# Performance work log

Measured on AMD Instinct MI355X. Metric: run time of the kernel, lower is better.

Reference implementation:

```python
import jax, jax.numpy as jnp
import numpy as np

N_FREQ = 12
NUM_LODS = 8
NUM_SAMPLED_LODS = 1
N_NEURONS = 64
OUT_CH = 11  # NUM_CANONICAL_CHANNELS = sum([3,3,1,1,1,1,1])
LRELU_SLOPE = 0.01
B = 1 << 20
# base_res = max_resolution >> (n_levels - 1); fpl = save_bits // quantize_bits = 4
GRIDS = [dict(base_res=16, n_levels=8, fpl=4),   # max_res 2048
         dict(base_res=16, n_levels=7, fpl=4)]   # max_res 1024


def _level_geom(base_res, level):
    # tcnn dense grid: scale = base_res * 2^level - 1, res = ceil(scale) + 1
    scale = base_res * (2.0 ** level) - 1.0
    res = int(np.ceil(scale)) + 1
    return res, scale


def _grid_n_params(g):
    return sum(_level_geom(g['base_res'], l)[0] ** 2 for l in range(g['n_levels'])) * g['fpl']


def triangle_wave(uv, n_freq):
    # tcnn TriangleWave: per dim, per frequency f: tri(x * 2^f), dim-major layout
    freqs = (2.0 ** jnp.arange(n_freq, dtype=jnp.float32))
    xf = uv[:, :, None] * freqs                      # [B, 2, F]
    t = jnp.abs(xf - jnp.floor(xf + 0.5)) * 4.0 - 1.0
    return t.reshape(uv.shape[0], -1)                # [B, 2*F]


def dense_grid_encode(uv, params_flat, base_res, n_levels, fpl):
    # Multi-level dense grid with bilinear interpolation (tcnn Grid/Dense/Linear).
    feats = []
    offset = 0
    for level in range(n_levels):
        res, scale = _level_geom(base_res, level)
        n = res * res * fpl
        table = params_flat[offset:offset + n].reshape(res * res, fpl)
        offset += n
        pos = uv * scale + 0.5                       # [B, 2]
        p0f = jnp.floor(pos)
        w = pos - p0f                                # bilinear weights
        p0 = jnp.clip(p0f.astype(jnp.int32), 0, res - 1)
        p1 = jnp.minimum(p0 + 1, res - 1)
        ix0, iy0 = p0[:, 0], p0[:, 1]
        ix1, iy1 = p1[:, 0], p1[:, 1]
        # tcnn index stride: dim0 fastest -> idx = ix + iy*res
        f00 = table[iy0 * res + ix0]
        f10 = table[iy0 * res + ix1]
        f01 = table[iy1 * res + ix0]
        f11 = table[iy1 * res + ix1]
        wx = w[:, 0:1]
        wy = w[:, 1:2]
        f = (f00 * (1 - wx) + f10 * wx) * (1 - wy) + (f01 * (1 - wx) + f11 * wx) * wy
        feats.append(f)                              # [B, fpl]
    return jnp.concatenate(feats, axis=1)            # [B, n_levels*fpl], level-major


def _forward(x, grid0_params, grid1_params, W_in, W_h, W_out):
    uvs = jnp.remainder(x[:, 0:2], 1.0)
    lod = x[:, 2:3]
    mips = lod * (NUM_LODS - NUM_SAMPLED_LODS)       # [B, 1]
    pe = triangle_wave(uvs, N_FREQ)                  # [B, 24]
    feats = []
    for g, params in zip(GRIDS, [grid0_params, grid1_params]):
        L, F = g['n_levels'], g['fpl']
        allf = dense_grid_encode(uvs, params, g['base_res'], L, F)  # [B, L*F]
        clipped = jnp.minimum(mips, float(L - NUM_SAMPLED_LODS))
        cols = ((L - NUM_SAMPLED_LODS - clipped) * F
                + jnp.arange(F * NUM_SAMPLED_LODS, dtype=jnp.float32)).astype(jnp.int32)
        feats.append(jnp.take_along_axis(allf, cols, axis=1))       # [B, F]
    inp = jnp.concatenate([pe] + feats + [lod], axis=1)             # [B, 33]
    lrelu = lambda h: jnp.where(h > 0, h, LRELU_SLOPE * h)
    h = lrelu(inp @ W_in)
    h = lrelu(h @ W_h)
    return lrelu(h @ W_out)                          # [B, 11]


def setup_inputs() -> dict:
    key = jax.random.key(0)
    ks = jax.random.split(key, 6)
    x = jax.random.uniform(ks[0], (B, 3), dtype=jnp.float32)
    grid0 = jax.random.uniform(ks[1], (_grid_n_params(GRIDS[0]),), jnp.float32, -0.1, 0.1)
    grid1 = jax.random.uniform(ks[2], (_grid_n_params(GRIDS[1]),), jnp.float32, -0.1, 0.1)
    n_in = N_FREQ * 2 + sum(g['fpl'] for g in GRIDS) * NUM_SAMPLED_LODS + 1
    W_in = jax.random.normal(ks[3], (n_in, N_NEURONS), jnp.float32) / np.float32(np.sqrt(n_in))
    W_h = jax.random.normal(ks[4], (N_NEURONS, N_NEURONS), jnp.float32) / np.float32(np.sqrt(N_NEURONS))
    W_out = jax.random.normal(ks[5], (N_NEURONS, OUT_CH), jnp.float32) / np.float32(np.sqrt(N_NEURONS))
    return dict(x=x, grid0_params=grid0, grid1_params=grid1, W_in=W_in, W_h=W_h, W_out=W_out)


def reference(x, grid0_params, grid1_params, W_in, W_h, W_out):
    return _forward(x, grid0_params, grid1_params, W_in, W_h, W_out)
```

## Files before the change

kernel.cpp:

```cpp
#include <hip/hip_runtime.h>

typedef float f32x4 __attribute__((ext_vector_type(4)));
typedef __bf16 bf16x8 __attribute__((ext_vector_type(8)));

#define PERM __builtin_amdgcn_perm

static __device__ __forceinline__ bf16x8 as_bf(uint4 v) {
    union { uint4 u; bf16x8 b; } c; c.u = v; return c.b;
}

static __device__ __forceinline__ float lrelu(float x) { return x > 0.0f ? x : 0.01f * x; }

static __device__ __forceinline__ unsigned pack_hilo(float v) {
    unsigned b = __float_as_uint(v);
    unsigned hi = (b + 0x7FFFu + ((b >> 16) & 1u)) >> 16;
    float hif = __uint_as_float(hi << 16);
    float lof = v - hif;
    unsigned lb = __float_as_uint(lof);
    unsigned lo = (lb + 0x7FFFu + ((lb >> 16) & 1u)) >> 16;
    return (hi << 16) | lo;
}

static __device__ __forceinline__ void unpack_frag(uint4 p0, uint4 p1, uint4& hi, uint4& lo) {
    hi.x = PERM(p0.y, p0.x, 0x07060302u);
    hi.y = PERM(p0.w, p0.z, 0x07060302u);
    hi.z = PERM(p1.y, p1.x, 0x07060302u);
    hi.w = PERM(p1.w, p1.z, 0x07060302u);
    lo.x = PERM(p0.y, p0.x, 0x05040100u);
    lo.y = PERM(p0.w, p0.z, 0x05040100u);
    lo.z = PERM(p1.y, p1.x, 0x05040100u);
    lo.w = PERM(p1.w, p1.z, 0x05040100u);
}

static __device__ __forceinline__ void read_frag_w(const unsigned* q, uint4& hi, uint4& lo) {
    uint4 p0 = *(const uint4*)(q);
    uint4 p1 = *(const uint4*)(q + 4);
    unpack_frag(p0, p1, hi, lo);
}

static __device__ __forceinline__ void read_frag_a(const unsigned* actb, int r, int kbase, int g,
                                                   uint4& hi, uint4& lo) {
    const unsigned* row = actb + r * 64;
    int cb = (kbase >> 2) + 2 * g;
    int rx = r & 15;
    uint4 p0 = *(const uint4*)(row + ((cb ^ rx) << 2));
    uint4 p1 = *(const uint4*)(row + (((cb + 1) ^ rx) << 2));
    unpack_frag(p0, p1, hi, lo);
}

static __device__ __forceinline__ void act_store(unsigned* actb, int row, int col, unsigned val) {
    int pos = row * 64 + ((((col >> 2) ^ (row & 15)) << 2) | (col & 3));
    actb[pos] = val;
}

static __device__ __forceinline__ f32x4 mfma3(const uint4& ah, const uint4& al,
                                              const uint4& bh, const uint4& bl, f32x4 c) {
    c = __builtin_amdgcn_mfma_f32_16x16x32_bf16(as_bf(ah), as_bf(bh), c, 0, 0, 0);
    c = __builtin_amdgcn_mfma_f32_16x16x32_bf16(as_bf(al), as_bf(bh), c, 0, 0, 0);
    c = __builtin_amdgcn_mfma_f32_16x16x32_bf16(as_bf(ah), as_bf(bl), c, 0, 0, 0);
    return c;
}

static __device__ __forceinline__ void issue_level(const float4* __restrict__ tbl, float u, float v,
                                                   int l, float4 r[4], float& wx, float& wy) {
    const int res = 16 << l;
    const float scale = (float)(res - 1);
    float px = u * scale + 0.5f;
    float py = v * scale + 0.5f;
    float fx = floorf(px), fy = floorf(py);
    wx = px - fx; wy = py - fy;
    int ix0 = min(max((int)fx, 0), res - 1);
    int iy0 = min(max((int)fy, 0), res - 1);
    int ix1 = min(ix0 + 1, res - 1);
    int iy1 = min(iy0 + 1, res - 1);
    unsigned base = (0x55555555u & ((1u << (2 * l)) - 1u)) * 256u;
    r[0] = tbl[base + iy0 * res + ix0];
    r[1] = tbl[base + iy0 * res + ix1];
    r[2] = tbl[base + iy1 * res + ix0];
    r[3] = tbl[base + iy1 * res + ix1];
}

static __device__ __forceinline__ void gather_issue(const float4* __restrict__ tbl, float u, float v,
                                                    float mips, float Lm1,
                                                    float4 r[8], float w[4], int cols[4]) {
    float clipped = fminf(mips, Lm1);
    float c0 = (Lm1 - clipped) * 4.0f;
    asm volatile("" : "+v"(c0));
    cols[0] = (int)c0;
    cols[1] = (int)(c0 + 1.0f);
    cols[2] = (int)(c0 + 2.0f);
    cols[3] = (int)(c0 + 3.0f);
    int lA = cols[0] >> 2;
    int lB = cols[3] >> 2;
    issue_level(tbl, u, v, lA, &r[0], w[0], w[1]);
    issue_level(tbl, u, v, lB, &r[4], w[2], w[3]);
}

static __device__ __forceinline__ void gather_finish(const float4 r[8], const float w[4],
                                                     const int cols[4], float out[4]) {
    float A[4], Bv[4];
    {
        float owx = 1.0f - w[0], owy = 1.0f - w[1];
        A[0] = (r[0].x * owx + r[1].x * w[0]) * owy + (r[2].x * owx + r[3].x * w[0]) * w[1];
        A[1] = (r[0].y * owx + r[1].y * w[0]) * owy + (r[2].y * owx + r[3].y * w[0]) * w[1];
        A[2] = (r[0].z * owx + r[1].z * w[0]) * owy + (r[2].z * owx + r[3].z * w[0]) * w[1];
        A[3] = (r[0].w * owx + r[1].w * w[0]) * owy + (r[2].w * owx + r[3].w * w[0]) * w[1];
    }
    {
        float owx = 1.0f - w[2], owy = 1.0f - w[3];
        Bv[0] = (r[4].x * owx + r[5].x * w[2]) * owy + (r[6].x * owx + r[7].x * w[2]) * w[3];
        Bv[1] = (r[4].y * owx + r[5].y * w[2]) * owy + (r[6].y * owx + r[7].y * w[2]) * w[3];
        Bv[2] = (r[4].z * owx + r[5].z * w[2]) * owy + (r[6].z * owx + r[7].z * w[2]) * w[3];
        Bv[3] = (r[4].w * owx + r[5].w * w[2]) * owy + (r[6].w * owx + r[7].w * w[2]) * w[3];
    }
    int lA = cols[0] >> 2;
    #pragma unroll
    for (int j = 0; j < 4; ++j) {
        int lj = cols[j] >> 2;
        int fj = cols[j] & 3;
        float va = A[0];
        va = (fj == 1) ? A[1] : va;
        va = (fj == 2) ? A[2] : va;
        va = (fj == 3) ? A[3] : va;
        float vb = Bv[0];
        vb = (fj == 1) ? Bv[1] : vb;
        vb = (fj == 2) ? Bv[2] : vb;
        vb = (fj == 3) ? Bv[3] : vb;
        out[j] = (lj == lA) ? va : vb;
    }
}

static __device__ __forceinline__ void pe_compute(float coord, unsigned pep[12]) {
    #pragma unroll
    for (int f = 0; f < 12; ++f) {
        float fr = (float)(1 << f);
        float xf = coord * fr;
        float t = fabsf(xf - floorf(xf + 0.5f)) * 4.0f - 1.0f;
        pep[f] = pack_hilo(t);
    }
}

#define LDS_U32 (2048 + 4096 + 1024 + 64 + 128 + 8192)

__global__ __launch_bounds__(256, 2) void tcnn_fwd(
    const float* __restrict__ x,
    const float4* __restrict__ g0,
    const float4* __restrict__ g1,
    const float* __restrict__ Win,
    const float* __restrict__ Wh,
    const float* __restrict__ Wout,
    float* __restrict__ out,
    int npts)
{
    extern __shared__ unsigned smem[];
    unsigned* s_winT  = smem;
    unsigned* s_whT   = s_winT + 2048;
    unsigned* s_woutT = s_whT + 4096;
    float*    s_lodw  = (float*)(s_woutT + 1024);
    float*    s_lodv  = s_lodw + 64;
    unsigned* s_act   = (unsigned*)(s_lodv + 128);

    const int tid = threadIdx.x;

    for (int e = tid; e < 2048; e += 256) {
        int n = e >> 5, k = e & 31;
        s_winT[n * 32 + k] = pack_hilo(Win[k * 64 + n]);
    }
    for (int e = tid; e < 4096; e += 256) {
        int n = e >> 6, k = e & 63;
        s_whT[n * 64 + k] = pack_hilo(Wh[k * 64 + n]);
    }
    for (int e = tid; e < 1024; e += 256) {
        int n = e >> 6, k = e & 63;
        float w = (n < 11) ? Wout[k * 11 + n] : 0.0f;
        s_woutT[n * 64 + k] = pack_hilo(w);
    }
    if (tid < 64) s_lodw[tid] = Win[32 * 64 + tid];
    __syncthreads();

    const int wv = tid >> 6;
    const int l = tid & 63;
    const int g = l >> 4;
    const int m = l & 15;
    const int half = l >> 5;
    const int p = l & 31;

    unsigned* act = s_act + wv * 2048;
    float* lodv = s_lodv + wv * 32;

    uint4 w1h[4], w1l[4];
    #pragma unroll
    for (int Nt = 0; Nt < 4; ++Nt)
        read_frag_w(s_winT + (Nt * 16 + m) * 32 + 8 * g, w1h[Nt], w1l[Nt]);
    uint4 w2h[4][2], w2l[4][2];
    #pragma unroll
    for (int Nt = 0; Nt < 4; ++Nt)
        #pragma unroll
        for (int ks = 0; ks < 2; ++ks)
            read_frag_w(s_whT + (Nt * 16 + m) * 64 + ks * 32 + 8 * g, w2h[Nt][ks], w2l[Nt][ks]);
    uint4 w3h[2], w3l[2];
    #pragma unroll
    for (int ks = 0; ks < 2; ++ks)
        read_frag_w(s_woutT + m * 64 + ks * 32 + 8 * g, w3h[ks], w3l[ks]);

    const float4* __restrict__ mytbl = half ? g1 : g0;
    const float myLm1 = half ? 6.0f : 7.0f;
    const int STRIDE = gridDim.x * 128;

    int cb0 = (blockIdx.x * 4 + wv) * 32;
    if (cb0 + 31 >= npts) return;

    unsigned pep[12], gfp[4];
    float lodcur;
    {
        int gp = cb0 + p;
        float xu = x[gp * 3 + 0];
        float xv = x[gp * 3 + 1];
        float xl = x[gp * 3 + 2];
        float u = xu - floorf(xu);
        float vv = xv - floorf(xv);
        pe_compute(half ? vv : u, pep);
        float4 r[8]; float wgt[4]; int cols[4];
        gather_issue(mytbl, u, vv, xl * 7.0f, myLm1, r, wgt, cols);
        float gf[4];
        gather_finish(r, wgt, cols, gf);
        #pragma unroll
        for (int j = 0; j < 4; ++j) gfp[j] = pack_hilo(gf[j]);
        lodcur = xl;
    }

    for (int cb = cb0; cb + 31 < npts; cb += STRIDE) {
        int next_cb = cb + STRIDE;
        if (next_cb + 31 >= npts) next_cb = cb;
        int gpn = next_cb + p;
        float xun = x[gpn * 3 + 0];
        float xvn = x[gpn * 3 + 1];
        float xln = x[gpn * 3 + 2];

        #pragma unroll
        for (int f = 0; f < 12; ++f) act_store(act, p, half * 12 + f, pep[f]);
        #pragma unroll
        for (int j = 0; j < 4; ++j) act_store(act, p, 24 + half * 4 + j, gfp[j]);
        if (half) lodv[p] = lodcur;
        __builtin_amdgcn_wave_barrier();

        uint4 a1h[2], a1l[2];
        #pragma unroll
        for (int Mt = 0; Mt < 2; ++Mt)
            read_frag_a(act, Mt * 16 + m, 0, g, a1h[Mt], a1l[Mt]);
        f32x4 acc1[2][4];
        #pragma unroll
        for (int Mt = 0; Mt < 2; ++Mt)
            #pragma unroll
            for (int Nt = 0; Nt < 4; ++Nt)
                acc1[Mt][Nt] = (f32x4){0.f, 0.f, 0.f, 0.f};
        #pragma unroll
        for (int Nt = 0; Nt < 4; ++Nt)
            #pragma unroll
            for (int Mt = 0; Mt < 2; ++Mt)
                acc1[Mt][Nt] = mfma3(a1h[Mt], a1l[Mt], w1h[Nt], w1l[Nt], acc1[Mt][Nt]);

        float un = xun - floorf(xun);
        float vvn = xvn - floorf(xvn);
        float4 r[8]; float wgt[4]; int cols[4];
        gather_issue(mytbl, un, vvn, xln * 7.0f, myLm1, r, wgt, cols);
        pe_compute(half ? vvn : un, pep);

        float lv[2][4];
        #pragma unroll
        for (int Mt = 0; Mt < 2; ++Mt)
            #pragma unroll
            for (int i = 0; i < 4; ++i)
                lv[Mt][i] = lodv[Mt * 16 + 4 * g + i];
        #pragma unroll
        for (int Nt = 0; Nt < 4; ++Nt) {
            float wl = s_lodw[Nt * 16 + m];
            #pragma unroll
            for (int Mt = 0; Mt < 2; ++Mt)
                #pragma unroll
                for (int i = 0; i < 4; ++i)
                    acc1[Mt][Nt][i] = fmaf(lv[Mt][i], wl, acc1[Mt][Nt][i]);
        }
        __builtin_amdgcn_wave_barrier();
        #pragma unroll
        for (int Mt = 0; Mt < 2; ++Mt)
            #pragma unroll
            for (int Nt = 0; Nt < 4; ++Nt)
                #pragma unroll
                for (int i = 0; i < 4; ++i)
                    act_store(act, Mt * 16 + 4 * g + i, Nt * 16 + m,
                              pack_hilo(lrelu(acc1[Mt][Nt][i])));
        __builtin_amdgcn_wave_barrier();

        f32x4 acc2[2][4];
        #pragma unroll
        for (int Mt = 0; Mt < 2; ++Mt)
            #pragma unroll
            for (int Nt = 0; Nt < 4; ++Nt)
                acc2[Mt][Nt] = (f32x4){0.f, 0.f, 0.f, 0.f};
        #pragma unroll
        for (int Mt = 0; Mt < 2; ++Mt) {
            uint4 ah[2], al[2];
            #pragma unroll
            for (int ks = 0; ks < 2; ++ks)
                read_frag_a(act, Mt * 16 + m, ks * 32, g, ah[ks], al[ks]);
            #pragma unroll
            for (int Nt = 0; Nt < 4; ++Nt)
                #pragma unroll
                for (int ks = 0; ks < 2; ++ks)
                    acc2[Mt][Nt] = mfma3(ah[ks], al[ks], w2h[Nt][ks], w2l[Nt][ks], acc2[Mt][Nt]);
        }
        __builtin_amdgcn_wave_barrier();
        #pragma unroll
        for (int Mt = 0; Mt < 2; ++Mt)
            #pragma unroll
            for (int Nt = 0; Nt < 4; ++Nt)
                #pragma unroll
                for (int i = 0; i < 4; ++i)
                    act_store(act, Mt * 16 + 4 * g + i, Nt * 16 + m,
                              pack_hilo(lrelu(acc2[Mt][Nt][i])));
        __builtin_amdgcn_wave_barrier();

        f32x4 acc3[2];
        acc3[0] = (f32x4){0.f, 0.f, 0.f, 0.f};
        acc3[1] = (f32x4){0.f, 0.f, 0.f, 0.f};
        #pragma unroll
        for (int Mt = 0; Mt < 2; ++Mt) {
            uint4 ah[2], al[2];
            #pragma unroll
            for (int ks = 0; ks < 2; ++ks)
                read_frag_a(act, Mt * 16 + m, ks * 32, g, ah[ks], al[ks]);
            #pragma unroll
            for (int ks = 0; ks < 2; ++ks)
                acc3[Mt] = mfma3(ah[ks], al[ks], w3h[ks], w3l[ks], acc3[Mt]);
        }
        #pragma unroll
        for (int Mt = 0; Mt < 2; ++Mt)
            #pragma unroll
            for (int i = 0; i < 4; ++i) {
                int row = Mt * 16 + 4 * g + i;
                float val = lrelu(acc3[Mt][i]);
                if (m < 11) out[(size_t)(cb + row) * 11 + m] = val;
            }
        __builtin_amdgcn_wave_barrier();

        float gf[4];
        gather_finish(r, wgt, cols, gf);
        #pragma unroll
        for (int j = 0; j < 4; ++j) gfp[j] = pack_hilo(gf[j]);
        lodcur = xln;
    }
}

extern "C" void kernel_launch(void* const* d_in, const int* in_sizes, int n_in,
                              void* d_out, int out_size, void* d_ws, size_t ws_size,
                              hipStream_t stream) {
    const float* x = (const float*)d_in[0];
    const float4* g0 = (const float4*)d_in[1];
    const float4* g1 = (const float4*)d_in[2];
    const float* Win = (const float*)d_in[3];
    const float* Wh = (const float*)d_in[4];
    const float* Wout = (const float*)d_in[5];
    float* out = (float*)d_out;
    int npts = in_sizes[0] / 3;
    tcnn_fwd<<<512, 256, LDS_U32 * 4, stream>>>(x, g0, g1, Win, Wh, Wout, out, npts);
}
```

Measured before the change: 306.4 us.

## Store activations and weights as separate bf16 hi/lo planes with swizzled LDS

Replaces the packed hi|lo 32-bit LDS layout, which needed perm unpacking on every fragment read, with separate hi and lo bf16 planes. MFMA fragments can now be loaded directly as bf16x8 vectors, and the splits use the paired float2-to-bf16x2 conversion. It also seeds the layer-1 accumulator with the LOD term instead of adding it after the MFMAs, and guards the prefetch with a precomputed trip count. The trade-off is extra 16-bit LDS stores and different bank-conflict behaviour from the new XOR swizzle.

```diff
diff --git a/kernel.cpp b/kernel.cpp
--- a/kernel.cpp
+++ b/kernel.cpp
@@ -1,63 +1,55 @@
 #include <hip/hip_runtime.h>
+#include <hip/hip_bf16.h>
 
 typedef float f32x4 __attribute__((ext_vector_type(4)));
 typedef __bf16 bf16x8 __attribute__((ext_vector_type(8)));
 
-#define PERM __builtin_amdgcn_perm
-
-static __device__ __forceinline__ bf16x8 as_bf(uint4 v) {
-    union { uint4 u; bf16x8 b; } c; c.u = v; return c.b;
-}
-
 static __device__ __forceinline__ float lrelu(float x) { return x > 0.0f ? x : 0.01f * x; }
 
-static __device__ __forceinline__ unsigned pack_hilo(float v) {
-    unsigned b = __float_as_uint(v);
-    unsigned hi = (b + 0x7FFFu + ((b >> 16) & 1u)) >> 16;
-    float hif = __uint_as_float(hi << 16);
-    float lof = v - hif;
-    unsigned lb = __float_as_uint(lof);
-    unsigned lo = (lb + 0x7FFFu + ((lb >> 16) & 1u)) >> 16;
-    return (hi << 16) | lo;
-}
-
-static __device__ __forceinline__ void unpack_frag(uint4 p0, uint4 p1, uint4& hi, uint4& lo) {
-    hi.x = PERM(p0.y, p0.x, 0x07060302u);
-    hi.y = PERM(p0.w, p0.z, 0x07060302u);
-    hi.z = PERM(p1.y, p1.x, 0x07060302u);
-    hi.w = PERM(p1.w, p1.z, 0x07060302u);
-    lo.x = PERM(p0.y, p0.x, 0x05040100u);
-    lo.y = PERM(p0.w, p0.z, 0x05040100u);
-    lo.z = PERM(p1.y, p1.x, 0x05040100u);
-    lo.w = PERM(p1.w, p1.z, 0x05040100u);
-}
-
-static __device__ __forceinline__ void read_frag_w(const unsigned* q, uint4& hi, uint4& lo) {
-    uint4 p0 = *(const uint4*)(q);
-    uint4 p1 = *(const uint4*)(q + 4);
-    unpack_frag(p0, p1, hi, lo);
-}
-
-static __device__ __forceinline__ void read_frag_a(const unsigned* actb, int r, int kbase, int g,
-                                                   uint4& hi, uint4& lo) {
-    const unsigned* row = actb + r * 64;
-    int cb = (kbase >> 2) + 2 * g;
-    int rx = r & 15;
-    uint4 p0 = *(const uint4*)(row + ((cb ^ rx) << 2));
-    uint4 p1 = *(const uint4*)(row + (((cb + 1) ^ rx) << 2));
-    unpack_frag(p0, p1, hi, lo);
-}
-
-static __device__ __forceinline__ void act_store(unsigned* actb, int row, int col, unsigned val) {
-    int pos = row * 64 + ((((col >> 2) ^ (row & 15)) << 2) | (col & 3));
-    actb[pos] = val;
-}
-
-static __device__ __forceinline__ f32x4 mfma3(const uint4& ah, const uint4& al,
-                                              const uint4& bh, const uint4& bl, f32x4 c) {
-    c = __builtin_amdgcn_mfma_f32_16x16x32_bf16(as_bf(ah), as_bf(bh), c, 0, 0, 0);
-    c = __builtin_amdgcn_mfma_f32_16x16x32_bf16(as_bf(al), as_bf(bh), c, 0, 0, 0);
-    c = __builtin_amdgcn_mfma_f32_16x16x32_bf16(as_bf(ah), as_bf(bl), c, 0, 0, 0);
+union bfu { __hip_bfloat162 b; unsigned u; };
+
+static __device__ __forceinline__ void split_pair(float a, float b, unsigned& hu, unsigned& lu) {
+    float2 f2; f2.x = a; f2.y = b;
+    bfu h; h.b = __float22bfloat162_rn(f2);
+    hu = h.u;
+    float2 r2;
+    r2.x = a - __uint_as_float(hu << 16);
+    r2.y = b - __uint_as_float(hu & 0xFFFF0000u);
+    bfu l; l.b = __float22bfloat162_rn(r2);
+    lu = l.u;
+}
+
+static __device__ __forceinline__ int swz64(int r, int k) {
+    return r * 64 + ((((k >> 3) ^ (r & 7)) << 3) | (k & 7));
+}
+static __device__ __forceinline__ int swz32(int r, int k) {
+    return r * 32 + ((((k >> 3) ^ (r & 3)) << 3) | (k & 7));
+}
+
+static __device__ __forceinline__ bf16x8 frag64(const unsigned short* pln, int r, int g2) {
+    return *(const bf16x8*)(pln + r * 64 + ((g2 ^ (r & 7)) << 3));
+}
+static __device__ __forceinline__ bf16x8 frag32(const unsigned short* pln, int r, int g2) {
+    return *(const bf16x8*)(pln + r * 32 + ((g2 ^ (r & 3)) << 3));
+}
+
+static __device__ __forceinline__ void store_k2(unsigned short* ph, unsigned short* pl,
+                                                int pos, float a, float b) {
+    unsigned hu, lu; split_pair(a, b, hu, lu);
+    *(unsigned*)(ph + pos) = hu;
+    *(unsigned*)(pl + pos) = lu;
+}
+static __device__ __forceinline__ void store_2(unsigned short* ph, unsigned short* pl,
+                                               int pos0, int pos1, float a, float b) {
+    unsigned hu, lu; split_pair(a, b, hu, lu);
+    ph[pos0] = (unsigned short)hu; ph[pos1] = (unsigned short)(hu >> 16);
+    pl[pos0] = (unsigned short)lu; pl[pos1] = (unsigned short)(lu >> 16);
+}
+
+static __device__ __forceinline__ f32x4 mfma3(bf16x8 ah, bf16x8 al, bf16x8 bh, bf16x8 bl, f32x4 c) {
+    c = __builtin_amdgcn_mfma_f32_16x16x32_bf16(ah, bh, c, 0, 0, 0);
+    c = __builtin_amdgcn_mfma_f32_16x16x32_bf16(al, bh, c, 0, 0, 0);
+    c = __builtin_amdgcn_mfma_f32_16x16x32_bf16(ah, bl, c, 0, 0, 0);
     return c;
 }
 
@@ -130,17 +122,16 @@
     }
 }
 
-static __device__ __forceinline__ void pe_compute(float coord, unsigned pep[12]) {
+static __device__ __forceinline__ void pe_compute(float coord, float pef[12]) {
     #pragma unroll
     for (int f = 0; f < 12; ++f) {
         float fr = (float)(1 << f);
         float xf = coord * fr;
-        float t = fabsf(xf - floorf(xf + 0.5f)) * 4.0f - 1.0f;
-        pep[f] = pack_hilo(t);
-    }
-}
-
-#define LDS_U32 (2048 + 4096 + 1024 + 64 + 128 + 8192)
+        pef[f] = fabsf(xf - floorf(xf + 0.5f)) * 4.0f - 1.0f;
+    }
+}
+
+#define LDS_BYTES ((64 + 128) * 4 + (2048 * 2 + 4096 * 2 + 1024 * 2 + 8192 * 2) * 2)
 
 __global__ __launch_bounds__(256, 2) void tcnn_fwd(
     const float* __restrict__ x,
@@ -152,28 +143,33 @@
     float* __restrict__ out,
     int npts)
 {
-    extern __shared__ unsigned smem[];
-    unsigned* s_winT  = smem;
-    unsigned* s_whT   = s_winT + 2048;
-    unsigned* s_woutT = s_whT + 4096;
-    float*    s_lodw  = (float*)(s_woutT + 1024);
-    float*    s_lodv  = s_lodw + 64;
-    unsigned* s_act   = (unsigned*)(s_lodv + 128);
+    extern __shared__ float smemf[];
+    float* s_lodw = smemf;
+    float* s_lodv = s_lodw + 64;
+    unsigned short* s_win_h = (unsigned short*)(s_lodv + 128);
+    unsigned short* s_win_l = s_win_h + 2048;
+    unsigned short* s_wh_h  = s_win_l + 2048;
+    unsigned short* s_wh_l  = s_wh_h + 4096;
+    unsigned short* s_wo_h  = s_wh_l + 4096;
+    unsigned short* s_wo_l  = s_wo_h + 1024;
+    unsigned short* s_act_h = s_wo_l + 1024;
+    unsigned short* s_act_l = s_act_h + 8192;
 
     const int tid = threadIdx.x;
 
-    for (int e = tid; e < 2048; e += 256) {
-        int n = e >> 5, k = e & 31;
-        s_winT[n * 32 + k] = pack_hilo(Win[k * 64 + n]);
-    }
-    for (int e = tid; e < 4096; e += 256) {
-        int n = e >> 6, k = e & 63;
-        s_whT[n * 64 + k] = pack_hilo(Wh[k * 64 + n]);
-    }
-    for (int e = tid; e < 1024; e += 256) {
-        int n = e >> 6, k = e & 63;
-        float w = (n < 11) ? Wout[k * 11 + n] : 0.0f;
-        s_woutT[n * 64 + k] = pack_hilo(w);
+    for (int q = tid; q < 1024; q += 256) {
+        int n = q >> 4, k0 = (q & 15) * 2;
+        store_k2(s_win_h, s_win_l, swz32(n, k0), Win[k0 * 64 + n], Win[(k0 + 1) * 64 + n]);
+    }
+    for (int q = tid; q < 2048; q += 256) {
+        int n = q >> 5, k0 = (q & 31) * 2;
+        store_k2(s_wh_h, s_wh_l, swz64(n, k0), Wh[k0 * 64 + n], Wh[(k0 + 1) * 64 + n]);
+    }
+    for (int q = tid; q < 512; q += 256) {
+        int n = q >> 5, k0 = (q & 31) * 2;
+        float a = (n < 11) ? Wout[k0 * 11 + n] : 0.0f;
+        float b = (n < 11) ? Wout[(k0 + 1) * 11 + n] : 0.0f;
+        store_k2(s_wo_h, s_wo_l, swz64(n, k0), a, b);
     }
     if (tid < 64) s_lodw[tid] = Win[32 * 64 + tid];
     __syncthreads();
@@ -185,23 +181,30 @@
     const int half = l >> 5;
     const int p = l & 31;
 
-    unsigned* act = s_act + wv * 2048;
+    unsigned short* act_h = s_act_h + wv * 2048;
+    unsigned short* act_l = s_act_l + wv * 2048;
     float* lodv = s_lodv + wv * 32;
 
-    uint4 w1h[4], w1l[4];
+    bf16x8 w1h[4], w1l[4];
+    #pragma unroll
+    for (int Nt = 0; Nt < 4; ++Nt) {
+        w1h[Nt] = frag32(s_win_h, Nt * 16 + m, g);
+        w1l[Nt] = frag32(s_win_l, Nt * 16 + m, g);
+    }
+    bf16x8 w2h[4][2], w2l[4][2];
     #pragma unroll
     for (int Nt = 0; Nt < 4; ++Nt)
-        read_frag_w(s_winT + (Nt * 16 + m) * 32 + 8 * g, w1h[Nt], w1l[Nt]);
-    uint4 w2h[4][2], w2l[4][2];
-    #pragma unroll
-    for (int Nt = 0; Nt < 4; ++Nt)
-        #pragma unroll
-        for (int ks = 0; ks < 2; ++ks)
-            read_frag_w(s_whT + (Nt * 16 + m) * 64 + ks * 32 + 8 * g, w2h[Nt][ks], w2l[Nt][ks]);
-    uint4 w3h[2], w3l[2];
-    #pragma unroll
-    for (int ks = 0; ks < 2; ++ks)
-        read_frag_w(s_woutT + m * 64 + ks * 32 + 8 * g, w3h[ks], w3l[ks]);
+        #pragma unroll
+        for (int ks = 0; ks < 2; ++ks) {
+            w2h[Nt][ks] = frag64(s_wh_h, Nt * 16 + m, ks * 4 + g);
+            w2l[Nt][ks] = frag64(s_wh_l, Nt * 16 + m, ks * 4 + g);
+        }
+    bf16x8 w3h[2], w3l[2];
+    #pragma unroll
+    for (int ks = 0; ks < 2; ++ks) {
+        w3h[ks] = frag64(s_wo_h, m, ks * 4 + g);
+        w3l[ks] = frag64(s_wo_l, m, ks * 4 + g);
+    }
 
     const float4* __restrict__ mytbl = half ? g1 : g0;
     const float myLm1 = half ? 6.0f : 7.0f;
@@ -209,8 +212,9 @@
 
     int cb0 = (blockIdx.x * 4 + wv) * 32;
     if (cb0 + 31 >= npts) return;
-
-    unsigned pep[12], gfp[4];
+    int nT = (npts - 32 - cb0) / STRIDE + 1;
+
+    float pef[12], gff[4];
     float lodcur;
     {
         int gp = cb0 + p;
@@ -219,59 +223,46 @@
         float xl = x[gp * 3 + 2];
         float u = xu - floorf(xu);
         float vv = xv - floorf(xv);
-        pe_compute(half ? vv : u, pep);
+        pe_compute(half ? vv : u, pef);
         float4 r[8]; float wgt[4]; int cols[4];
         gather_issue(mytbl, u, vv, xl * 7.0f, myLm1, r, wgt, cols);
-        float gf[4];
-        gather_finish(r, wgt, cols, gf);
-        #pragma unroll
-        for (int j = 0; j < 4; ++j) gfp[j] = pack_hilo(gf[j]);
+        gather_finish(r, wgt, cols, gff);
         lodcur = xl;
     }
 
-    for (int cb = cb0; cb + 31 < npts; cb += STRIDE) {
-        int next_cb = cb + STRIDE;
-        if (next_cb + 31 >= npts) next_cb = cb;
-        int gpn = next_cb + p;
-        float xun = x[gpn * 3 + 0];
-        float xvn = x[gpn * 3 + 1];
-        float xln = x[gpn * 3 + 2];
-
-        #pragma unroll
-        for (int f = 0; f < 12; ++f) act_store(act, p, half * 12 + f, pep[f]);
-        #pragma unroll
-        for (int j = 0; j < 4; ++j) act_store(act, p, 24 + half * 4 + j, gfp[j]);
+    for (int t = 0; t < nT; ++t) {
+        int cb = cb0 + t * STRIDE;
+        const bool pf = (t + 1 < nT);
+
+        float xun = 0.0f, xvn = 0.0f, xln = 0.0f;
+        if (pf) {
+            int gpn = cb + STRIDE + p;
+            xun = x[gpn * 3 + 0];
+            xvn = x[gpn * 3 + 1];
+            xln = x[gpn * 3 + 2];
+        }
+
+        #pragma unroll
+        for (int j = 0; j < 6; ++j)
+            store_k2(act_h, act_l, swz64(p, half * 12 + 2 * j), pef[2 * j], pef[2 * j + 1]);
+        store_k2(act_h, act_l, swz64(p, 24 + half * 4), gff[0], gff[1]);
+        store_k2(act_h, act_l, swz64(p, 24 + half * 4 + 2), gff[2], gff[3]);
         if (half) lodv[p] = lodcur;
         __builtin_amdgcn_wave_barrier();
 
-        uint4 a1h[2], a1l[2];
-        #pragma unroll
-        for (int Mt = 0; Mt < 2; ++Mt)
-            read_frag_a(act, Mt * 16 + m, 0, g, a1h[Mt], a1l[Mt]);
-        f32x4 acc1[2][4];
-        #pragma unroll
-        for (int Mt = 0; Mt < 2; ++Mt)
-            #pragma unroll
-            for (int Nt = 0; Nt < 4; ++Nt)
-                acc1[Mt][Nt] = (f32x4){0.f, 0.f, 0.f, 0.f};
-        #pragma unroll
-        for (int Nt = 0; Nt < 4; ++Nt)
-            #pragma unroll
-            for (int Mt = 0; Mt < 2; ++Mt)
-                acc1[Mt][Nt] = mfma3(a1h[Mt], a1l[Mt], w1h[Nt], w1l[Nt], acc1[Mt][Nt]);
-
-        float un = xun - floorf(xun);
-        float vvn = xvn - floorf(xvn);
-        float4 r[8]; float wgt[4]; int cols[4];
-        gather_issue(mytbl, un, vvn, xln * 7.0f, myLm1, r, wgt, cols);
-        pe_compute(half ? vvn : un, pep);
-
+        bf16x8 a1h[2], a1l[2];
+        #pragma unroll
+        for (int Mt = 0; Mt < 2; ++Mt) {
+            a1h[Mt] = frag64(act_h, Mt * 16 + m, g);
+            a1l[Mt] = frag64(act_l, Mt * 16 + m, g);
+        }
         float lv[2][4];
         #pragma unroll
         for (int Mt = 0; Mt < 2; ++Mt)
             #pragma unroll
             for (int i = 0; i < 4; ++i)
                 lv[Mt][i] = lodv[Mt * 16 + 4 * g + i];
+        f32x4 acc1[2][4];
         #pragma unroll
         for (int Nt = 0; Nt < 4; ++Nt) {
             float wl = s_lodw[Nt * 16 + m];
@@ -279,17 +270,34 @@
             for (int Mt = 0; Mt < 2; ++Mt)
                 #pragma unroll
                 for (int i = 0; i < 4; ++i)
-                    acc1[Mt][Nt][i] = fmaf(lv[Mt][i], wl, acc1[Mt][Nt][i]);
-        }
-        __builtin_amdgcn_wave_barrier();
-        #pragma unroll
-        for (int Mt = 0; Mt < 2; ++Mt)
-            #pragma unroll
-            for (int Nt = 0; Nt < 4; ++Nt)
-                #pragma unroll
-                for (int i = 0; i < 4; ++i)
-                    act_store(act, Mt * 16 + 4 * g + i, Nt * 16 + m,
-                              pack_hilo(lrelu(acc1[Mt][Nt][i])));
+                    acc1[Mt][Nt][i] = lv[Mt][i] * wl;
+        }
+        #pragma unroll
+        for (int Nt = 0; Nt < 4; ++Nt)
+            #pragma unroll
+            for (int Mt = 0; Mt < 2; ++Mt)
+                acc1[Mt][Nt] = mfma3(a1h[Mt], a1l[Mt], w1h[Nt], w1l[Nt], acc1[Mt][Nt]);
+
+        float4 r[8]; float wgt[4]; int cols[4];
+        float un = 0.0f, vvn = 0.0f;
+        if (pf) {
+            un = xun - floorf(xun);
+            vvn = xvn - floorf(xvn);
+            gather_issue(mytbl, un, vvn, xln * 7.0f, myLm1, r, wgt, cols);
+            pe_compute(half ? vvn : un, pef);
+        }
+
+        __builtin_amdgcn_wave_barrier();
+        #pragma unroll
+        for (int Mt = 0; Mt < 2; ++Mt)
+            #pragma unroll
+            for (int i = 0; i < 4; ++i) {
+                int row = Mt * 16 + 4 * g + i;
+                store_2(act_h, act_l, swz64(row, m), swz64(row, 16 + m),
+                        lrelu(acc1[Mt][0][i]), lrelu(acc1[Mt][1][i]));
+                store_2(act_h, act_l, swz64(row, 32 + m), swz64(row, 48 + m),
+                        lrelu(acc1[Mt][2][i]), lrelu(acc1[Mt][3][i]));
+            }
         __builtin_amdgcn_wave_barrier();
 
         f32x4 acc2[2][4];
@@ -300,10 +308,12 @@
                 acc2[Mt][Nt] = (f32x4){0.f, 0.f, 0.f, 0.f};
         #pragma unroll
         for (int Mt = 0; Mt < 2; ++Mt) {
-            uint4 ah[2], al[2];
-            #pragma unroll
-            for (int ks = 0; ks < 2; ++ks)
-                read_frag_a(act, Mt * 16 + m, ks * 32, g, ah[ks], al[ks]);
+            bf16x8 ah[2], al[2];
+            #pragma unroll
+            for (int ks = 0; ks < 2; ++ks) {
+                ah[ks] = frag64(act_h, Mt * 16 + m, ks * 4 + g);
+                al[ks] = frag64(act_l, Mt * 16 + m, ks * 4 + g);
+            }
             #pragma unroll
             for (int Nt = 0; Nt < 4; ++Nt)
                 #pragma unroll
@@ -314,11 +324,13 @@
         #pragma unroll
         for (int Mt = 0; Mt < 2; ++Mt)
             #pragma unroll
-            for (int Nt = 0; Nt < 4; ++Nt)
-                #pragma unroll
-                for (int i = 0; i < 4; ++i)
-                    act_store(act, Mt * 16 + 4 * g + i, Nt * 16 + m,
-                              pack_hilo(lrelu(acc2[Mt][Nt][i])));
+            for (int i = 0; i < 4; ++i) {
+                int row = Mt * 16 + 4 * g + i;
+                store_2(act_h, act_l, swz64(row, m), swz64(row, 16 + m),
+                        lrelu(acc2[Mt][0][i]), lrelu(acc2[Mt][1][i]));
+                store_2(act_h, act_l, swz64(row, 32 + m), swz64(row, 48 + m),
+                        lrelu(acc2[Mt][2][i]), lrelu(acc2[Mt][3][i]));
+            }
         __builtin_amdgcn_wave_barrier();
 
         f32x4 acc3[2];
@@ -326,10 +338,12 @@
         acc3[1] = (f32x4){0.f, 0.f, 0.f, 0.f};
         #pragma unroll
         for (int Mt = 0; Mt < 2; ++Mt) {
-            uint4 ah[2], al[2];
-            #pragma unroll
-            for (int ks = 0; ks < 2; ++ks)
-                read_frag_a(act, Mt * 16 + m, ks * 32, g, ah[ks], al[ks]);
+            bf16x8 ah[2], al[2];
+            #pragma unroll
+            for (int ks = 0; ks < 2; ++ks) {
+                ah[ks] = frag64(act_h, Mt * 16 + m, ks * 4 + g);
+                al[ks] = frag64(act_l, Mt * 16 + m, ks * 4 + g);
+            }
             #pragma unroll
             for (int ks = 0; ks < 2; ++ks)
                 acc3[Mt] = mfma3(ah[ks], al[ks], w3h[ks], w3l[ks], acc3[Mt]);
@@ -344,11 +358,10 @@
             }
         __builtin_amdgcn_wave_barrier();
 
-        float gf[4];
-        gather_finish(r, wgt, cols, gf);
-        #pragma unroll
-        for (int j = 0; j < 4; ++j) gfp[j] = pack_hilo(gf[j]);
-        lodcur = xln;
+        if (pf) {
+            gather_finish(r, wgt, cols, gff);
+            lodcur = xln;
+        }
     }
 }
 
@@ -363,5 +376,5 @@
     const float* Wout = (const float*)d_in[5];
     float* out = (float*)d_out;
     int npts = in_sizes[0] / 3;
-    tcnn_fwd<<<512, 256, LDS_U32 * 4, stream>>>(x, g0, g1, Win, Wh, Wout, out, npts);
-}
+    tcnn_fwd<<<512, 256, LDS_BYTES, stream>>>(x, g0, g1, Win, Wh, Wout, out, npts);
+}
```

Result: slower. 399.2 us (+30.3%).
